# Kernel tuning notes

Hardware: AMD Instinct MI355X
Metric: run time of the kernel (lower is better)

## Reference

```python
import jax, jax.numpy as jnp
import numpy as np

EMBED_DIM, KQ_DIM, V_DIM = 512, 64, 64
B, S = 2, 4096

def setup_inputs() -> dict:
    key = jax.random.key(0)
    k1, k2, k3, k4 = jax.random.split(key, 4)
    X = jax.random.normal(k1, (B, S, EMBED_DIM), dtype=jnp.float32)
    # nn.Linear(in, out, bias=False) weight has shape (out, in); y = x @ W.T
    Wq = jax.random.normal(k2, (KQ_DIM, EMBED_DIM), dtype=jnp.float32) * (EMBED_DIM ** -0.5)
    Wk = jax.random.normal(k3, (KQ_DIM, EMBED_DIM), dtype=jnp.float32) * (EMBED_DIM ** -0.5)
    Wv = jax.random.normal(k4, (V_DIM, EMBED_DIM), dtype=jnp.float32) * (EMBED_DIM ** -0.5)
    return {"X": X, "Wq": Wq, "Wk": Wk, "Wv": Wv}

def reference(X, Wq, Wk, Wv):
    # Q,K: [B,S,kq], V: [B,S,v]
    Q = jnp.einsum('bse,ke->bsk', X, Wq)
    K = jnp.einsum('bse,ke->bsk', X, Wk)
    V = jnp.einsum('bse,ve->bsv', X, Wv)
    scores = jnp.einsum('bqk,bsk->bqs', Q, K)  # [B,S,S]
    # FAITHFUL quirk: original divides by kq_dim**(-0.5) == multiply by sqrt(kq_dim)
    scaled = scores / (KQ_DIM ** -0.5)
    attn = jax.nn.softmax(scaled, axis=-1)
    context = jnp.einsum('bqs,bsv->bqv', attn, V)  # [B,S,v]
    return context
```

## Files before the change

kernel.cpp:

```cpp
#include <hip/hip_runtime.h>
#include <hip/hip_bf16.h>


typedef float  f32x16 __attribute__((ext_vector_type(16)));
typedef short  v8bf   __attribute__((ext_vector_type(8)));
typedef int    v4i    __attribute__((ext_vector_type(4)));

#define MFMA32(a, b, c) __builtin_amdgcn_mfma_f32_32x32x16_bf16((a), (b), (c), 0, 0, 0)

union Frag { v4i i4; v8bf b8; unsigned u[4]; };

__device__ __forceinline__ unsigned short f2bf(float x) {
    unsigned u = __float_as_uint(x);
    return (unsigned short)((u + 0x7fffu + ((u >> 16) & 1u)) >> 16);
}
__device__ __forceinline__ float bf2f(unsigned short h) {
    return __uint_as_float(((unsigned)h) << 16);
}
__device__ __forceinline__ unsigned cvt_pk_bf16(float a, float b) {
    unsigned r;
    asm("v_cvt_pk_bf16_f32 %0, %1, %2" : "=v"(r) : "v"(a), "v"(b));
    return r;
}


__global__ __launch_bounds__(256) void splitW_kernel(
    const float* __restrict__ wq, const float* __restrict__ wk, const float* __restrict__ wv,
    unsigned short* __restrict__ hi, unsigned short* __restrict__ lo)
{
    int i = blockIdx.x * 256 + threadIdx.x;
    int e = i * 4;
    const float* src = (e < 32768) ? wq : (e < 65536) ? wk : wv;
    int off = e & 32767;
    float4 v = *reinterpret_cast<const float4*>(src + off);
    unsigned short h0 = f2bf(v.x), h1 = f2bf(v.y), h2 = f2bf(v.z), h3 = f2bf(v.w);
    unsigned short l0 = f2bf(v.x - bf2f(h0)), l1 = f2bf(v.y - bf2f(h1));
    unsigned short l2 = f2bf(v.z - bf2f(h2)), l3 = f2bf(v.w - bf2f(h3));
    reinterpret_cast<uint2*>(hi)[i] =
        make_uint2((unsigned)h0 | ((unsigned)h1 << 16), (unsigned)h2 | ((unsigned)h3 << 16));
    reinterpret_cast<uint2*>(lo)[i] =
        make_uint2((unsigned)l0 | ((unsigned)l1 << 16), (unsigned)l2 | ((unsigned)l3 << 16));
}


__global__ __launch_bounds__(384, 1) void proj_kernel(
    const float* __restrict__ X,
    const unsigned short* __restrict__ Whi, const unsigned short* __restrict__ Wlo,
    unsigned short* __restrict__ Qhi, unsigned short* __restrict__ Qlo,
    unsigned short* __restrict__ Khi, unsigned short* __restrict__ Klo,
    unsigned short* __restrict__ VT)
{
    __shared__ uint4 XhiS[2048];
    __shared__ uint4 XloS[2048];
    __shared__ float t4[4][32][33];

    const int tid = threadIdx.x;
    const int w = tid >> 6;
    const int l = tid & 63, h = l >> 5, r32 = l & 31;
    const int row0 = blockIdx.x * 32;
    const int g = w >> 1, ct = w & 1;

    for (int id = tid; id < 2048; id += 384) {
        const int row = id >> 6, cc = id & 63;
        const float* xp = X + (row0 + row) * 512 + cc * 8;
        float4 va = *reinterpret_cast<const float4*>(xp);
        float4 vb = *reinterpret_cast<const float4*>(xp + 4);
        float xs[8] = {va.x, va.y, va.z, va.w, vb.x, vb.y, vb.z, vb.w};
        unsigned uh[4], ul[4];
#pragma unroll
        for (int j = 0; j < 4; ++j) {
            unsigned short h0 = f2bf(xs[2 * j]),            h1 = f2bf(xs[2 * j + 1]);
            unsigned short l0 = f2bf(xs[2 * j] - bf2f(h0)), l1 = f2bf(xs[2 * j + 1] - bf2f(h1));
            uh[j] = (unsigned)h0 | ((unsigned)h1 << 16);
            ul[j] = (unsigned)l0 | ((unsigned)l1 << 16);
        }
        const int idx = row * 64 + (cc ^ (row & 7));
        XhiS[idx] = make_uint4(uh[0], uh[1], uh[2], uh[3]);
        XloS[idx] = make_uint4(ul[0], ul[1], ul[2], ul[3]);
    }
    __syncthreads();

    f32x16 a0;
#pragma unroll
    for (int r = 0; r < 16; ++r) a0[r] = 0.f;

    for (int kc = 0; kc < 32; ++kc) {
        const int k0 = kc * 16 + 8 * h;
        const int idx = r32 * 64 + ((kc * 2 + h) ^ (r32 & 7));
        Frag xh, b0h;
        xh.i4 = *reinterpret_cast<const v4i*>(&XhiS[idx]);
        const int w0 = (g * 64 + ct * 32 + r32) * 512 + k0;
        b0h.i4 = *reinterpret_cast<const v4i*>(Whi + w0);
        a0 = MFMA32(xh.b8, b0h.b8, a0);
        if (g < 2) {
            Frag xl, b0l;
            xl.i4 = *reinterpret_cast<const v4i*>(&XloS[idx]);
            b0l.i4 = *reinterpret_cast<const v4i*>(Wlo + w0);
            a0 = MFMA32(xh.b8, b0l.b8, a0);
            a0 = MFMA32(xl.b8, b0h.b8, a0);
        }
    }

    const int bb = row0 >> 12;
    const int tl = (row0 & 4095) >> 5;

    if (g < 2) {
#pragma unroll
        for (int u = 0; u < 16; ++u)
            t4[w][(u & 3) + 8 * (u >> 2) + 4 * h][r32] = a0[u];
    }
    __syncthreads();

    if (g == 2) {
#pragma unroll
        for (int c = 0; c < 2; ++c)
#pragma unroll
            for (int hp = 0; hp < 2; ++hp) {
                unsigned p0 = (unsigned)f2bf(a0[8*c + 4*hp + 0]) |
                              ((unsigned)f2bf(a0[8*c + 4*hp + 1]) << 16);
                unsigned p1 = (unsigned)f2bf(a0[8*c + 4*hp + 2]) |
                              ((unsigned)f2bf(a0[8*c + 4*hp + 3]) << 16);
                const int off = ((((bb*128 + tl)*2 + c)*2 + ct)*64 + 32*hp + r32)*8 + 4*h;
                *reinterpret_cast<uint2*>(VT + off) = make_uint2(p0, p1);
            }
    } else if (g == 0) {
        unsigned wh[8], wl[8];
#pragma unroll
        for (int j = 0; j < 8; ++j) {
            float x0 = t4[w][r32][16 * h + 2 * j];
            float x1 = t4[w][r32][16 * h + 2 * j + 1];
            unsigned short h0 = f2bf(x0), h1 = f2bf(x1);
            unsigned short l0 = f2bf(x0 - bf2f(h0)), l1 = f2bf(x1 - bf2f(h1));
            wh[j] = (unsigned)h0 | ((unsigned)h1 << 16);
            wl[j] = (unsigned)l0 | ((unsigned)l1 << 16);
        }
        const int off = (row0 + r32) * 64 + ct * 32 + 16 * h;
        *reinterpret_cast<uint4*>(Qhi + off)     = make_uint4(wh[0], wh[1], wh[2], wh[3]);
        *reinterpret_cast<uint4*>(Qhi + off + 8) = make_uint4(wh[4], wh[5], wh[6], wh[7]);
        *reinterpret_cast<uint4*>(Qlo + off)     = make_uint4(wl[0], wl[1], wl[2], wl[3]);
        *reinterpret_cast<uint4*>(Qlo + off + 8) = make_uint4(wl[4], wl[5], wl[6], wl[7]);
    } else {
        const int dc = ct * 2 + h;
#pragma unroll
        for (int hp = 0; hp < 2; ++hp) {
            unsigned wh[4], wl[4];
#pragma unroll
            for (int jj = 0; jj < 4; ++jj) {
                float x0 = t4[w][r32][16 * h + 8 * hp + 2 * jj];
                float x1 = t4[w][r32][16 * h + 8 * hp + 2 * jj + 1];
                unsigned short h0 = f2bf(x0), h1 = f2bf(x1);
                unsigned short l0 = f2bf(x0 - bf2f(h0)), l1 = f2bf(x1 - bf2f(h1));
                wh[jj] = (unsigned)h0 | ((unsigned)h1 << 16);
                wl[jj] = (unsigned)l0 | ((unsigned)l1 << 16);
            }
            const int off = (((bb*128 + tl)*4 + dc)*64 + 32*hp + r32)*8;
            *reinterpret_cast<uint4*>(Khi + off) = make_uint4(wh[0], wh[1], wh[2], wh[3]);
            *reinterpret_cast<uint4*>(Klo + off) = make_uint4(wl[0], wl[1], wl[2], wl[3]);
        }
    }
}


__global__ __launch_bounds__(512, 2) void attn_kernel(
    const unsigned short* __restrict__ Qhi, const unsigned short* __restrict__ Qlo,
    const unsigned short* __restrict__ Khi, const unsigned short* __restrict__ Klo,
    const unsigned short* __restrict__ VT,
    float* __restrict__ Opart, float* __restrict__ ml)
{
    __shared__ float sO[8][32][68];
    __shared__ float sm[8][32];
    __shared__ float sl[8][32];

    const int tid = threadIdx.x;
    const int w = tid >> 6;
    const int l = tid & 63;
    const int h = l >> 5;
    const int q = l & 31;
    const int b  = blockIdx.x >> 7;
    const int q0 = (blockIdx.x & 127) * 32;
    const int half = blockIdx.y;

    Frag qh[4], ql[4];
#pragma unroll
    for (int dc = 0; dc < 4; ++dc) {
        const int o = (b * 4096 + q0 + q) * 64 + dc * 16 + 8 * h;
        qh[dc].i4 = *reinterpret_cast<const v4i*>(Qhi + o);
        ql[dc].i4 = *reinterpret_cast<const v4i*>(Qlo + o);
    }

    f32x16 o0, o1;
#pragma unroll
    for (int r = 0; r < 16; ++r) { o0[r] = 0.f; o1[r] = 0.f; }
    float m_run = -1e30f, l_run = 0.f;

    for (int it = 0; it < 4; ++it) {
        const int keyA = half * 2048 + (it * 16 + w) * 32;
        const int keyB = keyA + 256;
        const int tA = keyA >> 5;
        const int tB = keyB >> 5;

        f32x16 sA, sB;
#pragma unroll
        for (int r = 0; r < 16; ++r) { sA[r] = 0.f; sB[r] = 0.f; }
#pragma unroll
        for (int dc = 0; dc < 4; ++dc) {
            Frag kha, kla, khb, klb;
            const int koA = ((b * 128 + tA) * 4 + dc) * 512 + l * 8;
            const int koB = ((b * 128 + tB) * 4 + dc) * 512 + l * 8;
            kha.i4 = *reinterpret_cast<const v4i*>(Khi + koA);
            kla.i4 = *reinterpret_cast<const v4i*>(Klo + koA);
            khb.i4 = *reinterpret_cast<const v4i*>(Khi + koB);
            klb.i4 = *reinterpret_cast<const v4i*>(Klo + koB);
            sA = MFMA32(kha.b8, qh[dc].b8, sA);
            sB = MFMA32(khb.b8, qh[dc].b8, sB);
            sA = MFMA32(kha.b8, ql[dc].b8, sA);
            sB = MFMA32(khb.b8, ql[dc].b8, sB);
            sA = MFMA32(kla.b8, qh[dc].b8, sA);
            sB = MFMA32(klb.b8, qh[dc].b8, sB);
        }

        const float cc = 11.541560327111707f;
        float s2[32];
#pragma unroll
        for (int r = 0; r < 16; ++r) { s2[r] = sA[r] * cc; s2[16 + r] = sB[r] * cc; }
        float mb;
        {
            float t[8];
#pragma unroll
            for (int jj = 0; jj < 8; ++jj)
                t[jj] = fmaxf(fmaxf(s2[4 * jj], s2[4 * jj + 1]),
                              fmaxf(s2[4 * jj + 2], s2[4 * jj + 3]));
            float u0 = fmaxf(fmaxf(t[0], t[1]), fmaxf(t[2], t[3]));
            float u1 = fmaxf(fmaxf(t[4], t[5]), fmaxf(t[6], t[7]));
            mb = fmaxf(u0, u1);
        }
        mb = fmaxf(mb, __shfl_xor(mb, 32));

        const float m_new = fmaxf(m_run, mb);
        const float f = exp2f(m_run - m_new);
        float p[32];
        float ps0 = 0.f, ps1 = 0.f, ps2 = 0.f, ps3 = 0.f;
#pragma unroll
        for (int r = 0; r < 32; r += 4) {
            p[r]     = exp2f(s2[r]     - m_new); ps0 += p[r];
            p[r + 1] = exp2f(s2[r + 1] - m_new); ps1 += p[r + 1];
            p[r + 2] = exp2f(s2[r + 2] - m_new); ps2 += p[r + 2];
            p[r + 3] = exp2f(s2[r + 3] - m_new); ps3 += p[r + 3];
        }
        float ps = (ps0 + ps1) + (ps2 + ps3);
        ps += __shfl_xor(ps, 32);
        l_run = l_run * f + ps;
        m_run = m_new;
#pragma unroll
        for (int r = 0; r < 16; ++r) { o0[r] *= f; o1[r] *= f; }

        unsigned U[16];
#pragma unroll
        for (int j = 0; j < 8; ++j) {
            U[j]     = cvt_pk_bf16(p[2 * j],      p[2 * j + 1]);
            U[8 + j] = cvt_pk_bf16(p[16 + 2 * j], p[16 + 2 * j + 1]);
        }
        unsigned tA0 = h ? U[0]  : U[2];
        unsigned tA1 = h ? U[1]  : U[3];
        unsigned tA2 = h ? U[4]  : U[6];
        unsigned tA3 = h ? U[5]  : U[7];
        unsigned tB0 = h ? U[8]  : U[10];
        unsigned tB1 = h ? U[9]  : U[11];
        unsigned tB2 = h ? U[12] : U[14];
        unsigned tB3 = h ? U[13] : U[15];
        unsigned rA0 = __shfl_xor(tA0, 32);
        unsigned rA1 = __shfl_xor(tA1, 32);
        unsigned rA2 = __shfl_xor(tA2, 32);
        unsigned rA3 = __shfl_xor(tA3, 32);
        unsigned rB0 = __shfl_xor(tB0, 32);
        unsigned rB1 = __shfl_xor(tB1, 32);
        unsigned rB2 = __shfl_xor(tB2, 32);
        unsigned rB3 = __shfl_xor(tB3, 32);
        Frag p0f, p1f, p2f, p3f;
        if (h == 0) {
            p0f.u[0] = U[0];  p0f.u[1] = U[1];  p0f.u[2] = rA0;   p0f.u[3] = rA1;
            p1f.u[0] = U[4];  p1f.u[1] = U[5];  p1f.u[2] = rA2;   p1f.u[3] = rA3;
            p2f.u[0] = U[8];  p2f.u[1] = U[9];  p2f.u[2] = rB0;   p2f.u[3] = rB1;
            p3f.u[0] = U[12]; p3f.u[1] = U[13]; p3f.u[2] = rB2;   p3f.u[3] = rB3;
        } else {
            p0f.u[0] = rA0;   p0f.u[1] = rA1;   p0f.u[2] = U[2];  p0f.u[3] = U[3];
            p1f.u[0] = rA2;   p1f.u[1] = rA3;   p1f.u[2] = U[6];  p1f.u[3] = U[7];
            p2f.u[0] = rB0;   p2f.u[1] = rB1;   p2f.u[2] = U[10]; p2f.u[3] = U[11];
            p3f.u[0] = rB2;   p3f.u[1] = rB3;   p3f.u[2] = U[14]; p3f.u[3] = U[15];
        }

#pragma unroll
        for (int tb = 0; tb < 2; ++tb) {
            const int tt = tb ? tB : tA;
#pragma unroll
            for (int c = 0; c < 2; ++c) {
                const Frag& pf = tb ? (c ? p3f : p2f) : (c ? p1f : p0f);
#pragma unroll
                for (int vc = 0; vc < 2; ++vc) {
                    Frag vf;
                    const int vo = (((b * 128 + tt) * 2 + c) * 2 + vc) * 512 + l * 8;
                    vf.i4 = *reinterpret_cast<const v4i*>(VT + vo);
                    if (vc == 0) o0 = MFMA32(vf.b8, pf.b8, o0);
                    else         o1 = MFMA32(vf.b8, pf.b8, o1);
                }
            }
        }
    }

    if (h == 0) { sm[w][q] = m_run; sl[w][q] = l_run; }
#pragma unroll
    for (int vc = 0; vc < 2; ++vc) {
        const f32x16& a = vc ? o1 : o0;
#pragma unroll
        for (int u = 0; u < 4; ++u) {
            float4 v4 = make_float4(a[4 * u], a[4 * u + 1], a[4 * u + 2], a[4 * u + 3]);
            *reinterpret_cast<float4*>(&sO[w][q][vc * 32 + 8 * u + 4 * h]) = v4;
        }
    }
    __syncthreads();

    const int qq = tid >> 4;
    const int vb = (tid & 15) * 4;
    float mstar = sm[0][qq];
#pragma unroll
    for (int ww = 1; ww < 8; ++ww) mstar = fmaxf(mstar, sm[ww][qq]);
    float L = 0.f, acc0 = 0.f, acc1 = 0.f, acc2 = 0.f, acc3 = 0.f;
#pragma unroll
    for (int ww = 0; ww < 8; ++ww) {
        const float fw = exp2f(sm[ww][qq] - mstar);
        L += fw * sl[ww][qq];
        acc0 += fw * sO[ww][qq][vb + 0];
        acc1 += fw * sO[ww][qq][vb + 1];
        acc2 += fw * sO[ww][qq][vb + 2];
        acc3 += fw * sO[ww][qq][vb + 3];
    }
    const int row = b * 4096 + q0 + qq;
    *reinterpret_cast<float4*>(Opart + ((size_t)half * 8192 + row) * 64 + vb) =
        make_float4(acc0, acc1, acc2, acc3);
    if (vb == 0) {
        ml[((size_t)half * 8192 + row) * 2 + 0] = mstar;
        ml[((size_t)half * 8192 + row) * 2 + 1] = L;
    }
}

__global__ __launch_bounds__(256) void merge_kernel(
    const float* __restrict__ Opart, const float* __restrict__ ml, float* __restrict__ out)
{
    const int idx = blockIdx.x * 256 + threadIdx.x;
    const int row = idx >> 4, vb = (idx & 15) * 4;
    const float m0 = ml[row * 2 + 0],            l0 = ml[row * 2 + 1];
    const float m1 = ml[(8192 + row) * 2 + 0],   l1 = ml[(8192 + row) * 2 + 1];
    const float ms = fmaxf(m0, m1);
    const float w0 = exp2f(m0 - ms), w1 = exp2f(m1 - ms);
    const float inv = 1.0f / (w0 * l0 + w1 * l1);
    float4 a = *reinterpret_cast<const float4*>(Opart + (size_t)row * 64 + vb);
    float4 c = *reinterpret_cast<const float4*>(Opart + (size_t)(8192 + row) * 64 + vb);
    *reinterpret_cast<float4*>(out + (size_t)row * 64 + vb) =
        make_float4((w0 * a.x + w1 * c.x) * inv, (w0 * a.y + w1 * c.y) * inv,
                    (w0 * a.z + w1 * c.z) * inv, (w0 * a.w + w1 * c.w) * inv);
}


extern "C" void kernel_launch(void* const* d_in, const int* in_sizes, int n_in,
                              void* d_out, int out_size, void* d_ws, size_t ws_size,
                              hipStream_t stream)
{
    const float* X  = (const float*)d_in[0];
    const float* Wq = (const float*)d_in[1];
    const float* Wk = (const float*)d_in[2];
    const float* Wv = (const float*)d_in[3];
    float* out = (float*)d_out;

    unsigned short* Whi = (unsigned short*)d_ws;
    unsigned short* Wlo = Whi + 98304;
    unsigned short* Qhi = Wlo + 98304;
    unsigned short* Qlo = Qhi + 524288;
    unsigned short* Khi = Qlo + 524288;
    unsigned short* Klo = Khi + 524288;
    unsigned short* VT  = Klo + 524288;
    float* Opart = (float*)(VT + 524288);
    float* ml    = Opart + 1048576;

    splitW_kernel<<<96, 256, 0, stream>>>(Wq, Wk, Wv, Whi, Wlo);
    proj_kernel<<<256, 384, 0, stream>>>(X, Whi, Wlo, Qhi, Qlo, Khi, Klo, VT);
    attn_kernel<<<dim3(256, 2), 512, 0, stream>>>(Qhi, Qlo, Khi, Klo, VT, Opart, ml);
    merge_kernel<<<512, 256, 0, stream>>>(Opart, ml, out);
}
```

Before: 69.67 us.

## Fold softmax scale into Wq split and add lazy rescaling threshold

```diff
diff --git a/kernel.cpp b/kernel.cpp
--- a/kernel.cpp
+++ b/kernel.cpp
@@ -31,8 +31,10 @@
     int i = blockIdx.x * 256 + threadIdx.x;
     int e = i * 4;
     const float* src = (e < 32768) ? wq : (e < 65536) ? wk : wv;
+    const float sc = (e < 32768) ? 11.541560327111707f : 1.0f;
     int off = e & 32767;
     float4 v = *reinterpret_cast<const float4*>(src + off);
+    v.x *= sc; v.y *= sc; v.z *= sc; v.w *= sc;
     unsigned short h0 = f2bf(v.x), h1 = f2bf(v.y), h2 = f2bf(v.z), h3 = f2bf(v.w);
     unsigned short l0 = f2bf(v.x - bf2f(h0)), l1 = f2bf(v.y - bf2f(h1));
     unsigned short l2 = f2bf(v.z - bf2f(h2)), l3 = f2bf(v.w - bf2f(h3));
@@ -193,6 +195,7 @@
     for (int r = 0; r < 16; ++r) { o0[r] = 0.f; o1[r] = 0.f; }
     float m_run = -1e30f, l_run = 0.f;
 
+#pragma unroll 2
     for (int it = 0; it < 4; ++it) {
         const int keyA = half * 2048 + (it * 16 + w) * 32;
         const int keyB = keyA + 256;
@@ -219,40 +222,47 @@
             sB = MFMA32(klb.b8, qh[dc].b8, sB);
         }
 
-        const float cc = 11.541560327111707f;
-        float s2[32];
-#pragma unroll
-        for (int r = 0; r < 16; ++r) { s2[r] = sA[r] * cc; s2[16 + r] = sB[r] * cc; }
         float mb;
         {
             float t[8];
 #pragma unroll
-            for (int jj = 0; jj < 8; ++jj)
-                t[jj] = fmaxf(fmaxf(s2[4 * jj], s2[4 * jj + 1]),
-                              fmaxf(s2[4 * jj + 2], s2[4 * jj + 3]));
+            for (int jj = 0; jj < 4; ++jj) {
+                t[jj]     = fmaxf(fmaxf(sA[4 * jj], sA[4 * jj + 1]),
+                                  fmaxf(sA[4 * jj + 2], sA[4 * jj + 3]));
+                t[4 + jj] = fmaxf(fmaxf(sB[4 * jj], sB[4 * jj + 1]),
+                                  fmaxf(sB[4 * jj + 2], sB[4 * jj + 3]));
+            }
             float u0 = fmaxf(fmaxf(t[0], t[1]), fmaxf(t[2], t[3]));
             float u1 = fmaxf(fmaxf(t[4], t[5]), fmaxf(t[6], t[7]));
             mb = fmaxf(u0, u1);
         }
         mb = fmaxf(mb, __shfl_xor(mb, 32));
 
-        const float m_new = fmaxf(m_run, mb);
-        const float f = exp2f(m_run - m_new);
+        if (!__all(mb <= m_run + 8.f)) {
+            const float m_new = fmaxf(m_run, mb);
+            const float f = exp2f(m_run - m_new);
+#pragma unroll
+            for (int r = 0; r < 16; ++r) { o0[r] *= f; o1[r] *= f; }
+            l_run *= f;
+            m_run = m_new;
+        }
+
         float p[32];
         float ps0 = 0.f, ps1 = 0.f, ps2 = 0.f, ps3 = 0.f;
 #pragma unroll
-        for (int r = 0; r < 32; r += 4) {
-            p[r]     = exp2f(s2[r]     - m_new); ps0 += p[r];
-            p[r + 1] = exp2f(s2[r + 1] - m_new); ps1 += p[r + 1];
-            p[r + 2] = exp2f(s2[r + 2] - m_new); ps2 += p[r + 2];
-            p[r + 3] = exp2f(s2[r + 3] - m_new); ps3 += p[r + 3];
+        for (int r = 0; r < 16; r += 4) {
+            p[r]      = exp2f(sA[r]     - m_run); ps0 += p[r];
+            p[r + 1]  = exp2f(sA[r + 1] - m_run); ps1 += p[r + 1];
+            p[r + 2]  = exp2f(sA[r + 2] - m_run); ps2 += p[r + 2];
+            p[r + 3]  = exp2f(sA[r + 3] - m_run); ps3 += p[r + 3];
+            p[16 + r]     = exp2f(sB[r]     - m_run); ps0 += p[16 + r];
+            p[16 + r + 1] = exp2f(sB[r + 1] - m_run); ps1 += p[16 + r + 1];
+            p[16 + r + 2] = exp2f(sB[r + 2] - m_run); ps2 += p[16 + r + 2];
+            p[16 + r + 3] = exp2f(sB[r + 3] - m_run); ps3 += p[16 + r + 3];
         }
         float ps = (ps0 + ps1) + (ps2 + ps3);
         ps += __shfl_xor(ps, 32);
-        l_run = l_run * f + ps;
-        m_run = m_new;
-#pragma unroll
-        for (int r = 0; r < 16; ++r) { o0[r] *= f; o1[r] *= f; }
+        l_run += ps;
 
         unsigned U[16];
 #pragma unroll
```

Result: slower. 77.94 us (+11.9%).
